# Performance work log

Hardware: AMD Instinct MI355X
Metric: run time of the kernel (lower is better)

The kernel has to match this reference:

```python
import jax, jax.numpy as jnp
import numpy as np

EPS = 1e-5

def _inst_norm(x):
    # mean-variance normalization per (batch, channel) over spatial dims
    mu = jnp.mean(x, axis=(2, 3), keepdims=True)
    var = jnp.var(x, axis=(2, 3), keepdims=True)
    return (x - mu) / jnp.sqrt(var + EPS)

def _conv1x1(x, w, b):
    # x: (B,C,H,W), w: (O,C), b: (O,)
    return jnp.einsum('bchw,oc->bohw', x, w) + b[None, :, None, None]

def setup_inputs() -> dict:
    key = jax.random.key(0)
    ks = jax.random.split(key, 8)
    B, C, H, W = 16, 512, 64, 64
    f_c = jax.random.normal(ks[0], (B, C, H, W), dtype=jnp.float32)
    f_s = jax.random.normal(ks[1], (B, C, H, W), dtype=jnp.float32)
    w1 = jax.random.normal(ks[2], (C, C), dtype=jnp.float32) * 0.02
    b1 = jax.random.normal(ks[3], (C,), dtype=jnp.float32) * 0.02
    w2 = jax.random.normal(ks[4], (C, C), dtype=jnp.float32) * 0.02
    b2 = jax.random.normal(ks[5], (C,), dtype=jnp.float32) * 0.02
    w3 = jax.random.normal(ks[6], (C, C), dtype=jnp.float32) * 0.02
    b3 = jax.random.normal(ks[7], (C,), dtype=jnp.float32) * 0.02
    return {"f_c": f_c, "f_s": f_s, "w1": w1, "b1": b1, "w2": w2, "b2": b2, "w3": w3, "b3": b3}

def reference(f_c, f_s, w1, b1, w2, b2, w3, b3):
    b, c, h, w = f_c.shape
    f_c_norm = _inst_norm(f_c)
    f_s_norm = _inst_norm(f_s)
    fc = _conv1x1(f_c_norm, w1, b1).reshape(b, c, h * w)  # (B,C,HW)
    gs = _conv1x1(f_s_norm, w2, b2).reshape(b, c, h * w)  # (B,C,HW)
    hs = _conv1x1(f_s, w3, b3).reshape(b, c, h * w)       # (B,C,HW)
    # channel attention map (B,C,C) — softmax-free
    attn = jnp.einsum('bcn,bdn->bcd', gs, fc)
    out = jnp.einsum('bcd,bdn->bcn', attn, hs)
    return out.reshape(b, c, h, w)
```

## Files before the change

kernel.cpp:

```cpp
#include <hip/hip_runtime.h>
#include <hip/hip_bf16.h>

typedef float f4 __attribute__((ext_vector_type(4)));
typedef __bf16 bf16x4 __attribute__((ext_vector_type(4)));
typedef __bf16 bf16x8 __attribute__((ext_vector_type(8)));

#define BATCH 16
#define CCH 512
#define HW 4096

__device__ __forceinline__ void gld_lds16(const void* g, void* l) {
    __builtin_amdgcn_global_load_lds(
        (const __attribute__((address_space(1))) unsigned int*)g,
        (__attribute__((address_space(3))) unsigned int*)l, 16, 0, 0);
}

__global__ __launch_bounds__(256) void stats_conv_kernel(
    const float* __restrict__ fc, const float* __restrict__ fs,
    __bf16* __restrict__ fcb, __bf16* __restrict__ fsb,
    float* __restrict__ rstd_c, float* __restrict__ rmu_c,
    float* __restrict__ rstd_s, float* __restrict__ rmu_s)
{
    const int row = blockIdx.x;
    const float* pc = fc + (size_t)row * HW;
    const float* ps = fs + (size_t)row * HW;
    float sc = 0.f, qc = 0.f, ssum = 0.f, qs = 0.f;
    #pragma unroll
    for (int i0 = 0; i0 < HW / 8 / 256; i0++) {
        int i = i0 * 256 + threadIdx.x;
        f4 a0 = ((const f4*)pc)[2 * i], a1 = ((const f4*)pc)[2 * i + 1];
        f4 b0 = ((const f4*)ps)[2 * i], b1 = ((const f4*)ps)[2 * i + 1];
        #pragma unroll
        for (int t = 0; t < 4; t++) {
            sc += a0[t] + a1[t];
            qc = fmaf(a0[t], a0[t], fmaf(a1[t], a1[t], qc));
            ssum += b0[t] + b1[t];
            qs = fmaf(b0[t], b0[t], fmaf(b1[t], b1[t], qs));
        }
        if (fcb) {
            bf16x8 oa, ob;
            #pragma unroll
            for (int t = 0; t < 4; t++) {
                oa[t] = (__bf16)a0[t]; oa[4 + t] = (__bf16)a1[t];
                ob[t] = (__bf16)b0[t]; ob[4 + t] = (__bf16)b1[t];
            }
            *(bf16x8*)(fcb + (size_t)row * HW + i * 8) = oa;
            *(bf16x8*)(fsb + (size_t)row * HW + i * 8) = ob;
        }
    }
    for (int off = 32; off > 0; off >>= 1) {
        sc   += __shfl_down(sc,   off, 64);
        qc   += __shfl_down(qc,   off, 64);
        ssum += __shfl_down(ssum, off, 64);
        qs   += __shfl_down(qs,   off, 64);
    }
    __shared__ float red[4][4];
    if ((threadIdx.x & 63) == 0) {
        int w = threadIdx.x >> 6;
        red[w][0] = sc; red[w][1] = qc; red[w][2] = ssum; red[w][3] = qs;
    }
    __syncthreads();
    if (threadIdx.x == 0) {
        float Sc = red[0][0] + red[1][0] + red[2][0] + red[3][0];
        float Qc = red[0][1] + red[1][1] + red[2][1] + red[3][1];
        float Ss = red[0][2] + red[1][2] + red[2][2] + red[3][2];
        float Qs = red[0][3] + red[1][3] + red[2][3] + red[3][3];
        float muc = Sc * (1.f / HW), varc = Qc * (1.f / HW) - muc * muc;
        float mus = Ss * (1.f / HW), vars = Qs * (1.f / HW) - mus * mus;
        float rc = rsqrtf(varc + 1e-5f), rs = rsqrtf(vars + 1e-5f);
        rstd_c[row] = rc; rmu_c[row] = rc * muc;
        rstd_s[row] = rs; rmu_s[row] = rs * mus;
    }
}

__global__ __launch_bounds__(256) void prep_w_kernel(
    const float* __restrict__ w1, const float* __restrict__ w2, const float* __restrict__ w3,
    __bf16* __restrict__ w1t, __bf16* __restrict__ w2b, __bf16* __restrict__ w3t)
{
    int i = blockIdx.x * 256 + threadIdx.x;
    int z = blockIdx.y;
    if (z == 0)      w2b[i] = (__bf16)w2[i];
    else if (z == 1) w3t[i] = (__bf16)w3[(i & 511) * 512 + (i >> 9)];
    else             w1t[i] = (__bf16)w1[(i & 511) * 512 + (i >> 9)];
}

__global__ __launch_bounds__(256) void u_kernel(
    const float* __restrict__ w1, const float* __restrict__ b3,
    const float* __restrict__ w3, const float* __restrict__ b1,
    float* __restrict__ u1, float* __restrict__ bw3)
{
    int d = blockIdx.x * 256 + threadIdx.x;
    const float* W = blockIdx.y == 0 ? w1 : w3;
    const float* v = blockIdx.y == 0 ? b3 : b1;
    float* o       = blockIdx.y == 0 ? u1 : bw3;
    float s = 0.f;
    for (int x = 0; x < 512; x++) s += W[x * 512 + d] * v[x];
    o[d] = s;
}

__global__ __launch_bounds__(256) void b1b3_kernel(
    const float* __restrict__ b1, const float* __restrict__ b3, float* __restrict__ o)
{
    int t = threadIdx.x;
    float s = b1[t] * b3[t] + b1[t + 256] * b3[t + 256];
    for (int off = 32; off > 0; off >>= 1) s += __shfl_down(s, off, 64);
    __shared__ float ss[4];
    if ((t & 63) == 0) ss[t >> 6] = s;
    __syncthreads();
    if (t == 0) o[0] = ss[0] + ss[1] + ss[2] + ss[3];
}

__global__ __launch_bounds__(256) void gram_epi_kernel(
    const float* __restrict__ Graw, __bf16* __restrict__ G,
    const float* __restrict__ rstd_s, const float* __restrict__ rmu_s,
    const float* __restrict__ rstd_c, const float* __restrict__ rmu_c)
{
    size_t i4 = (size_t)blockIdx.x * 256 + threadIdx.x;
    size_t flat = i4 * 4;
    int b  = (int)(flat >> 18);
    int c  = (int)((flat >> 9) & 511);
    int d0 = (int)(flat & 511);
    float rs = rstd_s[b * 512 + c], rm = rmu_s[b * 512 + c];
    f4 g = *(const f4*)(Graw + flat);
    bf16x4 o;
    #pragma unroll
    for (int t = 0; t < 4; t++) {
        float val = rs * rstd_c[b * 512 + d0 + t] * g[t]
                  - 4096.f * rm * rmu_c[b * 512 + d0 + t];
        o[t] = (__bf16)val;
    }
    *(bf16x4*)(G + flat) = o;
}

__global__ __launch_bounds__(64) void q_kernel(
    const __bf16* __restrict__ G, const float* __restrict__ u1, float* __restrict__ q)
{
    int r = blockIdx.x;
    const __bf16* row = G + (size_t)r * 512;
    float s = 0.f;
    for (int i = threadIdx.x; i < 512; i += 64) s += (float)row[i] * u1[i];
    for (int off = 32; off > 0; off >>= 1) s += __shfl_down(s, off, 64);
    if (threadIdx.x == 0) q[r] = s;
}

__global__ __launch_bounds__(64) void v2_kernel(
    const float* __restrict__ w2, const float* __restrict__ qv,
    const float* __restrict__ b2, const float* __restrict__ b1b3,
    float* __restrict__ vv)
{
    int r = blockIdx.x, b = r >> 9, c = r & 511;
    float s = 0.f;
    for (int i = threadIdx.x; i < 512; i += 64) s += w2[c * 512 + i] * qv[b * 512 + i];
    for (int off = 32; off > 0; off >>= 1) s += __shfl_down(s, off, 64);
    if (threadIdx.x == 0) vv[r] = s + 4096.f * b1b3[0] * b2[c];
}

__global__ __launch_bounds__(256) void transpose_kernel(
    const __bf16* __restrict__ in, __bf16* __restrict__ out)
{
    __shared__ __align__(16) __bf16 t[64 * 64];
    const int b = blockIdx.z, e0 = blockIdx.y * 64, n0 = blockIdx.x * 64;
    const int tid = threadIdx.x;
    const __bf16* src = in + ((size_t)b * 512 + e0) * HW + n0;
    __bf16* dst = out + ((size_t)b * HW + n0) * 512 + e0;
    #pragma unroll
    for (int it = 0; it < 2; it++) {
        int idx = it * 256 + tid;
        int e = idx >> 3, v = idx & 7;
        *(bf16x8*)&t[e * 64 + ((v ^ (e & 7)) * 8)] =
            *(const bf16x8*)(src + (size_t)e * HW + v * 8);
    }
    __syncthreads();
    #pragma unroll
    for (int it = 0; it < 2; it++) {
        int idx = it * 256 + tid;
        int n = idx >> 3, v = idx & 7;
        bf16x8 o;
        #pragma unroll
        for (int u = 0; u < 8; u++) {
            int row = v * 8 + u;
            o[u] = t[row * 64 + (((n >> 3) ^ u) * 8) + (n & 7)];
        }
        *(bf16x8*)(dst + (size_t)n * 512 + v * 8) = o;
    }
}

template<int BM, int BN, bool D_F32, bool ATOMIC>
__global__ __launch_bounds__(256) void gemm_nt_lds(
    const __bf16* __restrict__ A, const __bf16* __restrict__ B, void* __restrict__ D,
    int K, int splitk, int lda, int ldb, int ldd,
    long long sA, long long sB, long long sD,
    const float* __restrict__ t1, int vt1, const float* __restrict__ t2, int vt2,
    float tscale)
{
    constexpr int FM = BM / 32, FN = BN / 32;
    __shared__ __align__(16) __bf16 As[BM * 64];
    __shared__ __align__(16) __bf16 Bs[BN * 64];

    const int tid = threadIdx.x;
    const int lane = tid & 63, wid = tid >> 6;
    const int b = blockIdx.z / splitk, chunk = blockIdx.z % splitk;
    const int klen = K / splitk, k0 = chunk * klen, k1 = k0 + klen;
    const int m0 = blockIdx.y * BM, n0 = blockIdx.x * BN;
    const int l16 = lane & 15, l4 = lane >> 4;
    const int wm = (wid >> 1) * (BM / 2), wn = (wid & 1) * (BN / 2);
    const int r_in = lane >> 3, slot = lane & 7;
    const int csw = (slot ^ r_in) * 8;
    const int rsw = (l16 & 7) * 8;

    const __bf16* Ab = A + (long long)b * sA;
    const __bf16* Bb = B + (long long)b * sB;

    f4 acc[FM][FN];
    #pragma unroll
    for (int i = 0; i < FM; i++)
        #pragma unroll
        for (int j = 0; j < FN; j++) acc[i][j] = (f4){0.f, 0.f, 0.f, 0.f};

    for (int kt = k0; kt < k1; kt += 64) {
        __syncthreads();
        #pragma unroll
        for (int i = 0; i < BM / 32; i++) {
            int ch = i * 4 + wid;
            gld_lds16(Ab + (long long)(m0 + ch * 8 + r_in) * lda + kt + csw,
                      As + ch * 512);
        }
        #pragma unroll
        for (int i = 0; i < BN / 32; i++) {
            int ch = i * 4 + wid;
            gld_lds16(Bb + (long long)(n0 + ch * 8 + r_in) * ldb + kt + csw,
                      Bs + ch * 512);
        }
        __syncthreads();
        #pragma unroll
        for (int kk = 0; kk < 2; kk++) {
            bf16x8 af[FM], bfr[FN];
            #pragma unroll
            for (int i = 0; i < FM; i++)
                af[i] = *(const bf16x8*)&As[(wm + i * 16 + l16) * 64 + ((kk * 32 + l4 * 8) ^ rsw)];
            #pragma unroll
            for (int j = 0; j < FN; j++)
                bfr[j] = *(const bf16x8*)&Bs[(wn + j * 16 + l16) * 64 + ((kk * 32 + l4 * 8) ^ rsw)];
            #pragma unroll
            for (int i = 0; i < FM; i++)
                #pragma unroll
                for (int j = 0; j < FN; j++)
                    acc[i][j] = __builtin_amdgcn_mfma_f32_16x16x32_bf16(af[i], bfr[j], acc[i][j], 0, 0, 0);
        }
    }

    char* Dbase = (char*)D + (long long)b * sD * (D_F32 ? 4 : 2);
    if (ATOMIC) {
        float* D32 = (float*)Dbase;
        #pragma unroll
        for (int j = 0; j < FN; j++) {
            int col = n0 + wn + j * 16 + l16;
            #pragma unroll
            for (int i = 0; i < FM; i++)
                #pragma unroll
                for (int rr = 0; rr < 4; rr++) {
                    int row = m0 + wm + i * 16 + l4 * 4 + rr;
                    atomicAdd(D32 + (size_t)row * ldd + col, acc[i][j][rr]);
                }
        }
        return;
    }
    const float* t1b = t1 ? t1 + (long long)b * vt1 : nullptr;
    const float* t2b = t2 ? t2 + (long long)b * vt2 : nullptr;
    #pragma unroll
    for (int j = 0; j < FN; j++) {
        int col = n0 + wn + j * 16 + l16;
        float ct = t2b ? t2b[col] : 1.f;
        #pragma unroll
        for (int i = 0; i < FM; i++) {
            #pragma unroll
            for (int rr = 0; rr < 4; rr++) {
                int row = m0 + wm + i * 16 + l4 * 4 + rr;
                float val = acc[i][j][rr];
                if (t1b) val += tscale * t1b[row] * ct;
                size_t idx = (size_t)row * ldd + col;
                if (D_F32) ((float*)Dbase)[idx] = val;
                else       ((__bf16*)Dbase)[idx] = (__bf16)val;
            }
        }
    }
}

template<int BM, int BN, bool A_F32, bool B_F32, bool B_KMAJOR, bool D_F32, bool ATOMIC>
__global__ __launch_bounds__(256) void gemm_kernel(
    const void* __restrict__ Ap, const void* __restrict__ Bp, void* __restrict__ Dp,
    int K, int splitk, int lda, int ldb, int ldd,
    long long sA, long long sB, long long sD,
    const float* __restrict__ s1, int vs1, const float* __restrict__ s2, int vs2,
    const float* __restrict__ t1, int vt1, const float* __restrict__ t2, int vt2,
    float tscale)
{
    static_assert(B_KMAJOR || BN == 128, "NN staging assumes BN=128");
    constexpr int FM = BM / 32, FN = BN / 32;
    constexpr int LSA = 40;
    constexpr int LSB = B_KMAJOR ? 40 : 36;
    __shared__ __bf16 As[BM * LSA];
    __shared__ __bf16 Bs[BN * LSB];

    const int tid = threadIdx.x;
    const int b = blockIdx.z / splitk;
    const int chunk = blockIdx.z % splitk;
    const int klen = K / splitk;
    const int k0 = chunk * klen, k1 = k0 + klen;
    const int m0 = blockIdx.y * BM, n0 = blockIdx.x * BN;
    const int lane = tid & 63, wid = tid >> 6;
    const int wm = (wid >> 1) * (BM / 2), wn = (wid & 1) * (BN / 2);
    const int l16 = lane & 15, l4 = lane >> 4;

    const char* Abase = (const char*)Ap + (long long)b * sA * (A_F32 ? 4 : 2);
    const char* Bbase = (const char*)Bp + (long long)b * sB * (B_F32 ? 4 : 2);
    char* Dbase = (char*)Dp + (long long)b * sD * (D_F32 ? 4 : 2);

    f4 acc[FM][FN];
    #pragma unroll
    for (int i = 0; i < FM; i++)
        #pragma unroll
        for (int j = 0; j < FN; j++) acc[i][j] = (f4){0.f, 0.f, 0.f, 0.f};

    for (int kt = k0; kt < k1; kt += 32) {
        __syncthreads();
        if (A_F32) {
            const float* A32 = (const float*)Abase;
            #pragma unroll
            for (int it = 0; it < BM / 32; it++) {
                int q = it * 256 + tid;
                int r = q >> 3, c = (q & 7) * 4;
                f4 v = *(const f4*)(A32 + (size_t)(m0 + r) * lda + kt + c);
                bf16x4 o;
                o[0] = (__bf16)v[0]; o[1] = (__bf16)v[1]; o[2] = (__bf16)v[2]; o[3] = (__bf16)v[3];
                *(bf16x4*)&As[r * LSA + c] = o;
            }
        } else {
            const __bf16* A16 = (const __bf16*)Abase;
            #pragma unroll
            for (int it = 0; it < BM / 64; it++) {
                int q = it * 256 + tid;
                int r = q >> 2, c = (q & 3) * 8;
                *(bf16x8*)&As[r * LSA + c] = *(const bf16x8*)(A16 + (size_t)(m0 + r) * lda + kt + c);
            }
        }
        if (B_KMAJOR) {
            if (B_F32) {
                const float* B32 = (const float*)Bbase;
                #pragma unroll
                for (int it = 0; it < BN / 32; it++) {
                    int q = it * 256 + tid;
                    int r = q >> 3, c = (q & 7) * 4;
                    f4 v = *(const f4*)(B32 + (size_t)(n0 + r) * ldb + kt + c);
                    bf16x4 o;
                    o[0] = (__bf16)v[0]; o[1] = (__bf16)v[1]; o[2] = (__bf16)v[2]; o[3] = (__bf16)v[3];
                    *(bf16x4*)&Bs[r * LSB + c] = o;
                }
            } else {
                const __bf16* B16 = (const __bf16*)Bbase;
                #pragma unroll
                for (int it = 0; it < BN / 64; it++) {
                    int q = it * 256 + tid;
                    int r = q >> 2, c = (q & 3) * 8;
                    *(bf16x8*)&Bs[r * LSB + c] = *(const bf16x8*)(B16 + (size_t)(n0 + r) * ldb + kt + c);
                }
            }
        } else {
            const int n = tid & 127;
            const int kh = (tid >> 7) * 4;
            #pragma unroll
            for (int kk = 0; kk < 32; kk += 8) {
                int k = kk + kh;
                bf16x4 o;
                if (B_F32) {
                    const float* B32 = (const float*)Bbase;
                    #pragma unroll
                    for (int t = 0; t < 4; t++)
                        o[t] = (__bf16)B32[(size_t)(kt + k + t) * ldb + n0 + n];
                } else {
                    const __bf16* B16 = (const __bf16*)Bbase;
                    #pragma unroll
                    for (int t = 0; t < 4; t++)
                        o[t] = B16[(size_t)(kt + k + t) * ldb + n0 + n];
                }
                *(bf16x4*)&Bs[n * LSB + k] = o;
            }
        }
        __syncthreads();

        bf16x8 af[FM], bfr[FN];
        #pragma unroll
        for (int i = 0; i < FM; i++)
            af[i] = *(const bf16x8*)&As[(wm + i * 16 + l16) * LSA + l4 * 8];
        #pragma unroll
        for (int j = 0; j < FN; j++) {
            if (B_KMAJOR) {
                bfr[j] = *(const bf16x8*)&Bs[(wn + j * 16 + l16) * LSB + l4 * 8];
            } else {
                const __bf16* p = &Bs[(wn + j * 16 + l16) * LSB + l4 * 8];
                bf16x4 lo = *(const bf16x4*)p;
                bf16x4 hi = *(const bf16x4*)(p + 4);
                bf16x8 r;
                r[0]=lo[0]; r[1]=lo[1]; r[2]=lo[2]; r[3]=lo[3];
                r[4]=hi[0]; r[5]=hi[1]; r[6]=hi[2]; r[7]=hi[3];
                bfr[j] = r;
            }
        }
        #pragma unroll
        for (int i = 0; i < FM; i++)
            #pragma unroll
            for (int j = 0; j < FN; j++)
                acc[i][j] = __builtin_amdgcn_mfma_f32_16x16x32_bf16(af[i], bfr[j], acc[i][j], 0, 0, 0);
    }

    if (ATOMIC) {
        float* D32 = (float*)Dbase;
        #pragma unroll
        for (int j = 0; j < FN; j++) {
            int col = n0 + wn + j * 16 + l16;
            #pragma unroll
            for (int i = 0; i < FM; i++)
                #pragma unroll
                for (int rr = 0; rr < 4; rr++) {
                    int row = m0 + wm + i * 16 + l4 * 4 + rr;
                    atomicAdd(D32 + (size_t)row * ldd + col, acc[i][j][rr]);
                }
        }
        return;
    }
    const float* s1b = s1 ? s1 + (long long)b * vs1 : nullptr;
    const float* s2b = s2 ? s2 + (long long)b * vs2 : nullptr;
    const float* t1b = t1 ? t1 + (long long)b * vt1 : nullptr;
    const float* t2b = t2 ? t2 + (long long)b * vt2 : nullptr;
    #pragma unroll
    for (int j = 0; j < FN; j++) {
        int col = n0 + wn + j * 16 + l16;
        float cs = s2b ? s2b[col] : 1.f;
        float ct = t2b ? t2b[col] : 1.f;
        #pragma unroll
        for (int i = 0; i < FM; i++) {
            #pragma unroll
            for (int rr = 0; rr < 4; rr++) {
                int row = m0 + wm + i * 16 + l4 * 4 + rr;
                float val = acc[i][j][rr];
                if (s1b) val *= s1b[row];
                val *= cs;
                if (t1b) val += tscale * t1b[row] * ct;
                size_t idx = (size_t)row * ldd + col;
                if (D_F32) ((float*)Dbase)[idx] = val;
                else       ((__bf16*)Dbase)[idx] = (__bf16)val;
            }
        }
    }
}

extern "C" void kernel_launch(void* const* d_in, const int* in_sizes, int n_in,
                              void* d_out, int out_size, void* d_ws, size_t ws_size,
                              hipStream_t stream) {
    (void)in_sizes; (void)n_in; (void)out_size;
    const float* f_c = (const float*)d_in[0];
    const float* f_s = (const float*)d_in[1];
    const float* w1  = (const float*)d_in[2];
    const float* b1  = (const float*)d_in[3];
    const float* w2  = (const float*)d_in[4];
    const float* b2  = (const float*)d_in[5];
    const float* w3  = (const float*)d_in[6];
    const float* b3  = (const float*)d_in[7];
    float* out = (float*)d_out;

    char* ws = (char*)d_ws;
    float*  rstd_c = (float*)(ws + 0);
    float*  rmu_c  = (float*)(ws + 32768);
    float*  rstd_s = (float*)(ws + 65536);
    float*  rmu_s  = (float*)(ws + 98304);
    float*  vvec   = (float*)(ws + 131072);
    float*  qvec   = (float*)(ws + 163840);
    float*  u1     = (float*)(ws + 196608);
    float*  bw3    = (float*)(ws + 198656);
    float*  b1b3p  = (float*)(ws + 200704);
    __bf16* w2b    = (__bf16*)(ws + 262144);
    __bf16* w1t    = (__bf16*)(ws + 786432);
    __bf16* w3t    = (__bf16*)(ws + 1310720);
    __bf16* w13t   = (__bf16*)(ws + 1835008);
    float*  Graw   = (float*)(ws + 2359296);
    __bf16* Pt     = (__bf16*)(ws + 2359296);
    __bf16* Mbuf   = (__bf16*)(ws + 10747904);
    __bf16* G      = (__bf16*)(ws + 19136512);
    __bf16* fcb    = (__bf16*)(ws + 27525120);
    __bf16* fst    = (__bf16*)(ws + 27525120);
    __bf16* fsb    = (__bf16*)(ws + 94633984);
    const bool CONV = ws_size >= (size_t)161742848;

    const long long sBig = (long long)CCH * HW;
    const long long sSm  = (long long)CCH * CCH;

    stats_conv_kernel<<<dim3(BATCH * CCH), 256, 0, stream>>>(
        f_c, f_s, CONV ? fcb : nullptr, CONV ? fsb : nullptr,
        rstd_c, rmu_c, rstd_s, rmu_s);
    prep_w_kernel<<<dim3(1024, 3), 256, 0, stream>>>(w1, w2, w3, w1t, w2b, w3t);
    u_kernel<<<dim3(2, 2), 256, 0, stream>>>(w1, b3, w3, b1, u1, bw3);
    b1b3_kernel<<<1, 256, 0, stream>>>(b1, b3, b1b3p);
    (void)hipMemsetAsync(Graw, 0, (size_t)16777216, stream);

    if (CONV)
        gemm_nt_lds<128, 128, true, true><<<dim3(4, 4, BATCH * 4), 256, 0, stream>>>(
            fsb, fcb, Graw, HW, 4, HW, HW, CCH, sBig, sBig, sSm,
            nullptr, 0, nullptr, 0, 0.f);
    else
        gemm_kernel<128,128,true,true,true,true,true><<<dim3(4, 4, BATCH * 4), 256, 0, stream>>>(
            f_s, f_c, Graw, HW, 4, HW, HW, CCH, sBig, sBig, sSm,
            nullptr,0, nullptr,0, nullptr,0, nullptr,0, 0.f);
    gram_epi_kernel<<<4096, 256, 0, stream>>>(Graw, G, rstd_s, rmu_s, rstd_c, rmu_c);

    if (CONV)
        transpose_kernel<<<dim3(64, 8, BATCH), 256, 0, stream>>>(fsb, fst);

    gemm_kernel<64,64,false,false,true,false,false><<<dim3(8, 8, 1), 256, 0, stream>>>(
        w3t, w1t, w13t, CCH, 1, CCH, CCH, CCH, 0, 0, 0,
        nullptr,0, nullptr,0, nullptr,0, nullptr,0, 0.f);
    gemm_nt_lds<128, 128, false, false><<<dim3(4, 4, BATCH), 256, 0, stream>>>(
        w13t, G, Pt, CCH, 1, CCH, CCH, CCH, 0, sSm, sSm,
        nullptr, 0, nullptr, 0, 0.f);
    gemm_nt_lds<128, 128, false, false><<<dim3(4, 4, BATCH), 256, 0, stream>>>(
        w2b, Pt, Mbuf, CCH, 1, CCH, CCH, CCH, 0, sSm, sSm,
        b2, 0, bw3, 0, 4096.f);

    q_kernel<<<BATCH * CCH, 64, 0, stream>>>(G, u1, qvec);
    v2_kernel<<<BATCH * CCH, 64, 0, stream>>>(w2, qvec, b2, b1b3p, vvec);

    if (CONV)
        gemm_nt_lds<128, 128, true, false><<<dim3(32, 4, BATCH), 256, 0, stream>>>(
            Mbuf, fst, out, CCH, 1, CCH, CCH, HW, sSm, sBig, sBig,
            vvec, CCH, nullptr, 0, 1.f);
    else
        gemm_kernel<128,128,false,true,false,true,false><<<dim3(32, 4, BATCH), 256, 0, stream>>>(
            Mbuf, f_s, out, CCH, 1, CCH, HW, HW, sSm, sBig, sBig,
            nullptr,0, nullptr,0, vvec,CCH, nullptr,0, 1.f);
}
```

Before: 627.4 us.

## Replace split-K atomics with partial slabs, fuse gram epilogue with q reduction

The split-K Gram GEMM now writes each K-chunk's partial result to a separate fp32 slab instead of using atomics on a memset buffer. A new per-row epilogue kernel sums the partials, applies the normalization correction, writes bf16 G and computes the q dot product in the same pass, which removes the memset, the atomics and the separate q_kernel. The change also retiles the two small 512x512 batched GEMMs to 64x64 for more blocks, adds nontemporal stores for the large fp32 output, and loads all inputs up front in the stats kernel. In exchange it needs an extra 48 MB of workspace and reads four partial buffers, and it falls back to the old path when the workspace is smaller.

```diff
diff --git a/kernel.cpp b/kernel.cpp
--- a/kernel.cpp
+++ b/kernel.cpp
@@ -22,31 +22,35 @@
     float* __restrict__ rstd_s, float* __restrict__ rmu_s)
 {
     const int row = blockIdx.x;
-    const float* pc = fc + (size_t)row * HW;
-    const float* ps = fs + (size_t)row * HW;
+    const int tid = threadIdx.x;
+    const f4* pc4 = (const f4*)(fc + (size_t)row * HW);
+    const f4* ps4 = (const f4*)(fs + (size_t)row * HW);
+    f4 av[4], bv[4];
+    av[0] = pc4[2 * tid];       av[1] = pc4[2 * tid + 1];
+    av[2] = pc4[2 * tid + 512]; av[3] = pc4[2 * tid + 513];
+    bv[0] = ps4[2 * tid];       bv[1] = ps4[2 * tid + 1];
+    bv[2] = ps4[2 * tid + 512]; bv[3] = ps4[2 * tid + 513];
     float sc = 0.f, qc = 0.f, ssum = 0.f, qs = 0.f;
     #pragma unroll
-    for (int i0 = 0; i0 < HW / 8 / 256; i0++) {
-        int i = i0 * 256 + threadIdx.x;
-        f4 a0 = ((const f4*)pc)[2 * i], a1 = ((const f4*)pc)[2 * i + 1];
-        f4 b0 = ((const f4*)ps)[2 * i], b1 = ((const f4*)ps)[2 * i + 1];
+    for (int u = 0; u < 4; u++)
         #pragma unroll
         for (int t = 0; t < 4; t++) {
-            sc += a0[t] + a1[t];
-            qc = fmaf(a0[t], a0[t], fmaf(a1[t], a1[t], qc));
-            ssum += b0[t] + b1[t];
-            qs = fmaf(b0[t], b0[t], fmaf(b1[t], b1[t], qs));
-        }
-        if (fcb) {
-            bf16x8 oa, ob;
-            #pragma unroll
-            for (int t = 0; t < 4; t++) {
-                oa[t] = (__bf16)a0[t]; oa[4 + t] = (__bf16)a1[t];
-                ob[t] = (__bf16)b0[t]; ob[4 + t] = (__bf16)b1[t];
-            }
-            *(bf16x8*)(fcb + (size_t)row * HW + i * 8) = oa;
-            *(bf16x8*)(fsb + (size_t)row * HW + i * 8) = ob;
-        }
+            sc += av[u][t];  qc = fmaf(av[u][t], av[u][t], qc);
+            ssum += bv[u][t]; qs = fmaf(bv[u][t], bv[u][t], qs);
+        }
+    if (fcb) {
+        bf16x8 o0, o1, p0, p1;
+        #pragma unroll
+        for (int t = 0; t < 4; t++) {
+            o0[t] = (__bf16)av[0][t]; o0[4 + t] = (__bf16)av[1][t];
+            o1[t] = (__bf16)av[2][t]; o1[4 + t] = (__bf16)av[3][t];
+            p0[t] = (__bf16)bv[0][t]; p0[4 + t] = (__bf16)bv[1][t];
+            p1[t] = (__bf16)bv[2][t]; p1[4 + t] = (__bf16)bv[3][t];
+        }
+        *(bf16x8*)(fcb + (size_t)row * HW + 8 * tid)         = o0;
+        *(bf16x8*)(fcb + (size_t)row * HW + 8 * (256 + tid)) = o1;
+        *(bf16x8*)(fsb + (size_t)row * HW + 8 * tid)         = p0;
+        *(bf16x8*)(fsb + (size_t)row * HW + 8 * (256 + tid)) = p1;
     }
     for (int off = 32; off > 0; off >>= 1) {
         sc   += __shfl_down(sc,   off, 64);
@@ -55,12 +59,12 @@
         qs   += __shfl_down(qs,   off, 64);
     }
     __shared__ float red[4][4];
-    if ((threadIdx.x & 63) == 0) {
-        int w = threadIdx.x >> 6;
+    if ((tid & 63) == 0) {
+        int w = tid >> 6;
         red[w][0] = sc; red[w][1] = qc; red[w][2] = ssum; red[w][3] = qs;
     }
     __syncthreads();
-    if (threadIdx.x == 0) {
+    if (tid == 0) {
         float Sc = red[0][0] + red[1][0] + red[2][0] + red[3][0];
         float Qc = red[0][1] + red[1][1] + red[2][1] + red[3][1];
         float Ss = red[0][2] + red[1][2] + red[2][2] + red[3][2];
@@ -110,6 +114,45 @@
     if (t == 0) o[0] = ss[0] + ss[1] + ss[2] + ss[3];
 }
 
+template<int NP>
+__global__ __launch_bounds__(128) void gram_epi_q_kernel(
+    const float* __restrict__ P0, const float* __restrict__ P1,
+    const float* __restrict__ P2, const float* __restrict__ P3,
+    __bf16* __restrict__ G, const float* __restrict__ u1,
+    const float* __restrict__ rstd_s, const float* __restrict__ rmu_s,
+    const float* __restrict__ rstd_c, const float* __restrict__ rmu_c,
+    float* __restrict__ q)
+{
+    const int row = blockIdx.x;
+    const int b = row >> 9;
+    const int t = threadIdx.x;
+    const int d0 = t * 4;
+    const size_t flat = (size_t)row * 512 + d0;
+    f4 g = *(const f4*)(P0 + flat);
+    if (NP == 4) {
+        g += *(const f4*)(P1 + flat);
+        g += *(const f4*)(P2 + flat);
+        g += *(const f4*)(P3 + flat);
+    }
+    const float rs = rstd_s[row], rm = rmu_s[row];
+    const float* rc  = rstd_c + b * 512;
+    const float* rmc = rmu_c  + b * 512;
+    bf16x4 o;
+    float qp = 0.f;
+    #pragma unroll
+    for (int k = 0; k < 4; k++) {
+        float val = rs * rc[d0 + k] * g[k] - 4096.f * rm * rmc[d0 + k];
+        o[k] = (__bf16)val;
+        qp = fmaf((float)o[k], u1[d0 + k], qp);
+    }
+    *(bf16x4*)(G + flat) = o;
+    for (int off = 32; off > 0; off >>= 1) qp += __shfl_down(qp, off, 64);
+    __shared__ float sred[2];
+    if ((t & 63) == 0) sred[t >> 6] = qp;
+    __syncthreads();
+    if (t == 0) q[row] = sred[0] + sred[1];
+}
+
 __global__ __launch_bounds__(256) void gram_epi_kernel(
     const float* __restrict__ Graw, __bf16* __restrict__ G,
     const float* __restrict__ rstd_s, const float* __restrict__ rmu_s,
@@ -130,6 +173,7 @@
         o[t] = (__bf16)val;
     }
     *(bf16x4*)(G + flat) = o;
+    (void)c;
 }
 
 __global__ __launch_bounds__(64) void q_kernel(
@@ -185,13 +229,13 @@
     }
 }
 
-template<int BM, int BN, bool D_F32, bool ATOMIC>
+template<int BM, int BN, bool D_F32, bool ATOMIC, bool PARTIAL, bool NTSTORE>
 __global__ __launch_bounds__(256) void gemm_nt_lds(
     const __bf16* __restrict__ A, const __bf16* __restrict__ B, void* __restrict__ D,
     int K, int splitk, int lda, int ldb, int ldd,
     long long sA, long long sB, long long sD,
     const float* __restrict__ t1, int vt1, const float* __restrict__ t2, int vt2,
-    float tscale)
+    float tscale, float* __restrict__ Dalt, long long altStride)
 {
     constexpr int FM = BM / 32, FN = BN / 32;
     __shared__ __align__(16) __bf16 As[BM * 64];
@@ -249,6 +293,22 @@
         }
     }
 
+    if (PARTIAL) {
+        float* base = (chunk == 0) ? (float*)D : (Dalt + (long long)(chunk - 1) * altStride);
+        base += (long long)b * sD;
+        #pragma unroll
+        for (int j = 0; j < FN; j++) {
+            int col = n0 + wn + j * 16 + l16;
+            #pragma unroll
+            for (int i = 0; i < FM; i++)
+                #pragma unroll
+                for (int rr = 0; rr < 4; rr++) {
+                    int row = m0 + wm + i * 16 + l4 * 4 + rr;
+                    base[(size_t)row * ldd + col] = acc[i][j][rr];
+                }
+        }
+        return;
+    }
     char* Dbase = (char*)D + (long long)b * sD * (D_F32 ? 4 : 2);
     if (ATOMIC) {
         float* D32 = (float*)Dbase;
@@ -279,8 +339,12 @@
                 float val = acc[i][j][rr];
                 if (t1b) val += tscale * t1b[row] * ct;
                 size_t idx = (size_t)row * ldd + col;
-                if (D_F32) ((float*)Dbase)[idx] = val;
-                else       ((__bf16*)Dbase)[idx] = (__bf16)val;
+                if (D_F32) {
+                    if (NTSTORE) __builtin_nontemporal_store(val, (float*)Dbase + idx);
+                    else         ((float*)Dbase)[idx] = val;
+                } else {
+                    ((__bf16*)Dbase)[idx] = (__bf16)val;
+                }
             }
         }
     }
@@ -489,10 +553,13 @@
     __bf16* fcb    = (__bf16*)(ws + 27525120);
     __bf16* fst    = (__bf16*)(ws + 27525120);
     __bf16* fsb    = (__bf16*)(ws + 94633984);
-    const bool CONV = ws_size >= (size_t)161742848;
+    float*  slab   = (float*)(ws + 161742848);
+    const bool CONV  = ws_size >= (size_t)161742848;
+    const bool BIGWS = ws_size >= (size_t)161742848 + (size_t)3 * 16777216;
 
     const long long sBig = (long long)CCH * HW;
     const long long sSm  = (long long)CCH * CCH;
+    const long long sPart = (long long)BATCH * CCH * CCH;
 
     stats_conv_kernel<<<dim3(BATCH * CCH), 256, 0, stream>>>(
         f_c, f_s, CONV ? fcb : nullptr, CONV ? fsb : nullptr,
@@ -500,17 +567,30 @@
     prep_w_kernel<<<dim3(1024, 3), 256, 0, stream>>>(w1, w2, w3, w1t, w2b, w3t);
     u_kernel<<<dim3(2, 2), 256, 0, stream>>>(w1, b3, w3, b1, u1, bw3);
     b1b3_kernel<<<1, 256, 0, stream>>>(b1, b3, b1b3p);
-    (void)hipMemsetAsync(Graw, 0, (size_t)16777216, stream);
-
-    if (CONV)
-        gemm_nt_lds<128, 128, true, true><<<dim3(4, 4, BATCH * 4), 256, 0, stream>>>(
+
+    if (CONV && BIGWS) {
+        gemm_nt_lds<128, 128, true, false, true, false><<<dim3(4, 4, BATCH * 4), 256, 0, stream>>>(
             fsb, fcb, Graw, HW, 4, HW, HW, CCH, sBig, sBig, sSm,
-            nullptr, 0, nullptr, 0, 0.f);
-    else
+            nullptr, 0, nullptr, 0, 0.f, slab, sPart);
+        gram_epi_q_kernel<4><<<BATCH * CCH, 128, 0, stream>>>(
+            Graw, slab, slab + sPart, slab + 2 * sPart,
+            G, u1, rstd_s, rmu_s, rstd_c, rmu_c, qvec);
+    } else if (CONV) {
+        (void)hipMemsetAsync(Graw, 0, (size_t)16777216, stream);
+        gemm_nt_lds<128, 128, true, true, false, false><<<dim3(4, 4, BATCH * 4), 256, 0, stream>>>(
+            fsb, fcb, Graw, HW, 4, HW, HW, CCH, sBig, sBig, sSm,
+            nullptr, 0, nullptr, 0, 0.f, nullptr, 0);
+        gram_epi_q_kernel<1><<<BATCH * CCH, 128, 0, stream>>>(
+            Graw, nullptr, nullptr, nullptr,
+            G, u1, rstd_s, rmu_s, rstd_c, rmu_c, qvec);
+    } else {
+        (void)hipMemsetAsync(Graw, 0, (size_t)16777216, stream);
         gemm_kernel<128,128,true,true,true,true,true><<<dim3(4, 4, BATCH * 4), 256, 0, stream>>>(
             f_s, f_c, Graw, HW, 4, HW, HW, CCH, sBig, sBig, sSm,
             nullptr,0, nullptr,0, nullptr,0, nullptr,0, 0.f);
-    gram_epi_kernel<<<4096, 256, 0, stream>>>(Graw, G, rstd_s, rmu_s, rstd_c, rmu_c);
+        gram_epi_kernel<<<4096, 256, 0, stream>>>(Graw, G, rstd_s, rmu_s, rstd_c, rmu_c);
+        q_kernel<<<BATCH * CCH, 64, 0, stream>>>(G, u1, qvec);
+    }
 
     if (CONV)
         transpose_kernel<<<dim3(64, 8, BATCH), 256, 0, stream>>>(fsb, fst);
@@ -518,20 +598,19 @@
     gemm_kernel<64,64,false,false,true,false,false><<<dim3(8, 8, 1), 256, 0, stream>>>(
         w3t, w1t, w13t, CCH, 1, CCH, CCH, CCH, 0, 0, 0,
         nullptr,0, nullptr,0, nullptr,0, nullptr,0, 0.f);
-    gemm_nt_lds<128, 128, false, false><<<dim3(4, 4, BATCH), 256, 0, stream>>>(
+    gemm_nt_lds<64, 64, false, false, false, false><<<dim3(8, 8, BATCH), 256, 0, stream>>>(
         w13t, G, Pt, CCH, 1, CCH, CCH, CCH, 0, sSm, sSm,
-        nullptr, 0, nullptr, 0, 0.f);
-    gemm_nt_lds<128, 128, false, false><<<dim3(4, 4, BATCH), 256, 0, stream>>>(
+        nullptr, 0, nullptr, 0, 0.f, nullptr, 0);
+    gemm_nt_lds<64, 64, false, false, false, false><<<dim3(8, 8, BATCH), 256, 0, stream>>>(
         w2b, Pt, Mbuf, CCH, 1, CCH, CCH, CCH, 0, sSm, sSm,
-        b2, 0, bw3, 0, 4096.f);
-
-    q_kernel<<<BATCH * CCH, 64, 0, stream>>>(G, u1, qvec);
+        b2, 0, bw3, 0, 4096.f, nullptr, 0);
+
     v2_kernel<<<BATCH * CCH, 64, 0, stream>>>(w2, qvec, b2, b1b3p, vvec);
 
     if (CONV)
-        gemm_nt_lds<128, 128, true, false><<<dim3(32, 4, BATCH), 256, 0, stream>>>(
+        gemm_nt_lds<128, 128, true, false, false, true><<<dim3(32, 4, BATCH), 256, 0, stream>>>(
             Mbuf, fst, out, CCH, 1, CCH, CCH, HW, sSm, sBig, sBig,
-            vvec, CCH, nullptr, 0, 1.f);
+            vvec, CCH, nullptr, 0, 1.f, nullptr, 0);
     else
         gemm_kernel<128,128,false,true,false,true,false><<<dim3(32, 4, BATCH), 256, 0, stream>>>(
             Mbuf, f_s, out, CCH, 1, CCH, HW, HW, sSm, sBig, sBig,
```

Result: faster. 573.2 us (-8.6%).
